# Kernel optimization log

Hardware: AMD Instinct MI355X
Metric: run time of the kernel (lower is better)

## Reference

```python
import jax, jax.numpy as jnp
import numpy as np

N = 50000      # nodes
E = 1600000    # edges (avg degree 32)
F_IN = 512     # num_node_features
NHID = 128     # args.nhid
NCLS = 64      # num_classes


def _gcn_conv(x, W, b, src, dst):
    """PyG GCNConv with symmetric normalization and self-loops.
    x' = D^{-1/2} (A + I) D^{-1/2} (x W) + b, D = degree of (A + I)."""
    h = x @ W                                   # [N, d_out] linear first
    ones = jnp.ones(src.shape[0], h.dtype)
    deg = jnp.zeros(N, h.dtype).at[dst].add(ones) + 1.0  # +1 for self-loop
    dinv = jax.lax.rsqrt(deg)                   # D^{-1/2}
    norm = dinv[src] * dinv[dst]                # per-edge coefficient
    msg = h[src] * norm[:, None]                # gather + scale  [E, d_out]
    agg = jnp.zeros_like(h).at[dst].add(msg)    # scatter-add
    agg = agg + h * (dinv * dinv)[:, None]      # self-loop term (norm = dinv_i^2)
    return agg + b


def setup_inputs() -> dict:
    key = jax.random.key(0)
    k0, k1, k2, k3, k4, k5 = jax.random.split(key, 6)
    x = jax.random.normal(k0, (N, F_IN), jnp.float32)
    edge_index = jax.random.randint(k1, (2, E), 0, N, jnp.int32)
    W1 = jax.random.normal(k2, (F_IN, NHID), jnp.float32) / np.sqrt(F_IN)
    b1 = jnp.zeros((NHID,), jnp.float32)
    W2 = jax.random.normal(k3, (NHID, NCLS), jnp.float32) / np.sqrt(NHID)
    b2 = jnp.zeros((NCLS,), jnp.float32)
    return {"x": x, "edge_index": edge_index, "W1": W1, "b1": b1, "W2": W2, "b2": b2}


def reference(x, edge_index, W1, b1, W2, b2):
    src, dst = edge_index[0], edge_index[1]
    h = jax.nn.relu(_gcn_conv(x, W1, b1, src, dst))
    # dropout is identity at inference (training=False)
    out = _gcn_conv(h, W2, b2, src, dst)
    return jax.nn.softmax(out, axis=1)
```

## Files before the change

### kernel.cpp

```cpp
#include <hip/hip_runtime.h>
#include <hip/hip_bf16.h>
#include <hip/hip_fp16.h>


#define F_IN 512
#define NHID 128
#define NCLS 64
#define BSHIFT 8
#define CHUNK 4096
#define BM 64
#define BK 32

typedef __attribute__((ext_vector_type(8))) short short8;
typedef __attribute__((ext_vector_type(4))) float f32x4;

__device__ __forceinline__ unsigned f2u(float f) { union { float f; unsigned u; } v; v.f = f; return v.u; }
__device__ __forceinline__ float u2f(unsigned u) { union { unsigned u; float f; } v; v.u = u; return v.f; }


__global__ __launch_bounds__(256) void bin_kernel(const int* __restrict__ src,
        const int* __restrict__ dst, int2* __restrict__ pairs,
        int* __restrict__ bcur, int E, int cap) {
    __shared__ int lcnt[256];
    __shared__ int lscan[256];
    __shared__ int gbase[256];
    __shared__ int wsum[4];
    __shared__ int2 stage[CHUNK];
    const int t = threadIdx.x;
    const int lane = t & 63, wid = t >> 6;
    const int e0 = blockIdx.x * CHUNK;
    const int n = min(CHUNK, E - e0);

    lcnt[t] = 0;
    __syncthreads();
    for (int i = t; i < n; i += 256)
        atomicAdd(&lcnt[dst[e0 + i] >> BSHIFT], 1);
    __syncthreads();
    const int v = lcnt[t];
    int s = v;
    #pragma unroll
    for (int d = 1; d < 64; d <<= 1) {
        int tt = __shfl_up(s, d);
        if (lane >= d) s += tt;
    }
    if (lane == 63) wsum[wid] = s;
    __syncthreads();
    int woff = 0;
    for (int w = 0; w < wid; ++w) woff += wsum[w];
    lscan[t] = woff + s - v;
    gbase[t] = v ? atomicAdd(&bcur[t], v) : 0;
    lcnt[t] = 0;
    __syncthreads();
    for (int i = t; i < n; i += 256) {
        int d = dst[e0 + i], sc = src[e0 + i];
        int b = d >> BSHIFT;
        int p = atomicAdd(&lcnt[b], 1);
        stage[lscan[b] + p] = make_int2(d, sc);
    }
    __syncthreads();
    for (int i = t; i < n; i += 256) {
        int2 pr = stage[i];
        int b = pr.x >> BSHIFT;
        int off = gbase[b] + (i - lscan[b]);
        if (off < cap) pairs[(size_t)b * cap + off] = pr;
    }
}


__global__ __launch_bounds__(256) void count_b_kernel(const int2* __restrict__ pairs,
        const int* __restrict__ bcur, int* __restrict__ cnt, int cap) {
    __shared__ int hist[256];
    const int b = blockIdx.x;
    const int t = threadIdx.x;
    hist[t] = 0;
    __syncthreads();
    const int n = min(bcur[b], cap);
    const int2* p = pairs + (size_t)b * cap;
    for (int i = t; i < n; i += 256)
        atomicAdd(&hist[p[i].x & 255], 1);
    __syncthreads();
    cnt[(b << BSHIFT) + t] = hist[t];
}


__global__ __launch_bounds__(256) void scan1_kernel(const int* __restrict__ cnt,
        int* __restrict__ row_ptr, float* __restrict__ dinv,
        int* __restrict__ bsum, int N) {
    __shared__ int wsum[4];
    const int tid = threadIdx.x;
    const int lane = tid & 63, wid = tid >> 6;
    const int base = blockIdx.x * 1024 + tid * 4;
    int4 v = {0, 0, 0, 0};
    if (base + 3 < N) {
        v = *reinterpret_cast<const int4*>(&cnt[base]);
    } else {
        if (base + 0 < N) v.x = cnt[base + 0];
        if (base + 1 < N) v.y = cnt[base + 1];
        if (base + 2 < N) v.z = cnt[base + 2];
        if (base + 3 < N) v.w = cnt[base + 3];
    }
    if (base + 0 < N) dinv[base + 0] = rsqrtf((float)v.x + 1.0f);
    if (base + 1 < N) dinv[base + 1] = rsqrtf((float)v.y + 1.0f);
    if (base + 2 < N) dinv[base + 2] = rsqrtf((float)v.z + 1.0f);
    if (base + 3 < N) dinv[base + 3] = rsqrtf((float)v.w + 1.0f);
    const int tsum = v.x + v.y + v.z + v.w;
    int s = tsum;
    #pragma unroll
    for (int d = 1; d < 64; d <<= 1) {
        int t = __shfl_up(s, d);
        if (lane >= d) s += t;
    }
    if (lane == 63) wsum[wid] = s;
    __syncthreads();
    int woff = 0;
    for (int w = 0; w < wid; ++w) woff += wsum[w];
    const int excl = woff + s - tsum;
    if (base + 0 < N) row_ptr[base + 0] = excl;
    if (base + 1 < N) row_ptr[base + 1] = excl + v.x;
    if (base + 2 < N) row_ptr[base + 2] = excl + v.x + v.y;
    if (base + 3 < N) row_ptr[base + 3] = excl + v.x + v.y + v.z;
    if (tid == 255) bsum[blockIdx.x] = excl + tsum;
}

__global__ __launch_bounds__(64) void scan2_kernel(const int* __restrict__ bsum,
        int* __restrict__ boff, int* __restrict__ row_ptr, int nb, int N) {
    const int lane = threadIdx.x;
    int v = (lane < nb) ? bsum[lane] : 0;
    int s = v;
    #pragma unroll
    for (int d = 1; d < 64; d <<= 1) {
        int t = __shfl_up(s, d);
        if (lane >= d) s += t;
    }
    if (lane < nb) boff[lane] = s - v;
    if (lane == 63) row_ptr[N] = s;
}

__global__ void scan3_kernel(int* __restrict__ row_ptr, const int* __restrict__ boff, int N) {
    int i = blockIdx.x * blockDim.x + threadIdx.x;
    if (i < N) row_ptr[i] += boff[i >> 10];
}


__global__ __launch_bounds__(512) void fill_b_kernel(const int2* __restrict__ pairs,
        const int* __restrict__ bcur, const int* __restrict__ row_ptr,
        int* __restrict__ col, int cap) {
    __shared__ int lcur[256];
    const int b = blockIdx.x;
    const int t = threadIdx.x;
    if (t < 256) lcur[t] = 0;
    __syncthreads();
    const int n = min(bcur[b], cap);
    const int2* p = pairs + (size_t)b * cap;
    for (int i = t; i < n; i += 512) {
        int2 pr = p[i];
        int pos = row_ptr[pr.x] + atomicAdd(&lcur[pr.x & 255], 1);
        col[pos] = pr.y;
    }
}


__global__ __launch_bounds__(256) void prepW_kernel(const float* __restrict__ W1,
        short* __restrict__ Wp) {
    const int g = blockIdx.x * 256 + threadIdx.x;
    const int f = g >> 6;
    const int lane = g & 63;
    const int ks = f >> 3, nt = f & 7;
    const int colg = nt * 16 + (lane & 15);
    const int k0 = ks * 32 + (lane >> 4) * 8;
    short8 vb;
    #pragma unroll
    for (int j = 0; j < 8; ++j) {
        unsigned u = f2u(W1[(size_t)(k0 + j) * NHID + colg]);
        unsigned r = (u + 0x7fffu + ((u >> 16) & 1u)) >> 16;
        vb[j] = (short)r;
    }
    *reinterpret_cast<short8*>(Wp + ((size_t)f << 9) + (lane << 3)) = vb;
}


__device__ __forceinline__ void cvt8v(const f32x4& u0, const f32x4& u1,
                                      short8& h, short8& l) {
    float av[8] = {u0[0], u0[1], u0[2], u0[3], u1[0], u1[1], u1[2], u1[3]};
    #pragma unroll
    for (int j = 0; j < 8; ++j) {
        unsigned u = f2u(av[j]);
        h[j] = (short)(u >> 16);
        float hif = u2f(u & 0xffff0000u);
        l[j] = (short)(f2u(av[j] - hif) >> 16);
    }
}

#define STAGE(bufidx, ksv) do { \
    const char* _xb = (const char*)X + (size_t)(ksv) * 128; \
    char* _ab = (char*)&Abuf[bufidx][0] + tid * 16; \
    __builtin_amdgcn_global_load_lds((const unsigned*)(_xb + aoff0), (unsigned*)(_ab),        16, 0, 0); \
    __builtin_amdgcn_global_load_lds((const unsigned*)(_xb + aoff1), (unsigned*)(_ab + 4096), 16, 0, 0); \
    const char* _wb = (const char*)Wp + (size_t)(ksv) * 8192 + tid * 16; \
    char* _bb = (char*)&Bbuf[bufidx][0] + tid * 16; \
    __builtin_amdgcn_global_load_lds((const unsigned*)(_wb),        (unsigned*)(_bb),        16, 0, 0); \
    __builtin_amdgcn_global_load_lds((const unsigned*)(_wb + 4096), (unsigned*)(_bb + 4096), 16, 0, 0); \
} while (0)

__global__ __launch_bounds__(256, 4) void gemm1_mfma(
        const float* __restrict__ X, const short* __restrict__ Wp,
        const float* __restrict__ dinv, __half* __restrict__ Hs16, int M) {
    __shared__ float Abuf[2][BM * BK];
    __shared__ short Bbuf[2][8 * 512];
    const int tid = threadIdx.x;
    const int lane = tid & 63;
    const int wid = tid >> 6;
    const int l15 = lane & 15;
    const int kc = lane >> 4;
    const int m0 = blockIdx.x * BM;

    int aoff0, aoff1;
    {
        int o, row, c, grow;
        o = tid * 16;        row = o >> 7; c = ((o >> 4) & 7) ^ (row & 7);
        grow = m0 + row; if (grow > M - 1) grow = M - 1; aoff0 = grow * 2048 + c * 16;
        o = 4096 + tid * 16; row = o >> 7; c = ((o >> 4) & 7) ^ (row & 7);
        grow = m0 + row; if (grow > M - 1) grow = M - 1; aoff1 = grow * 2048 + c * 16;
    }

    const int row0 = wid * 16 + l15;
    const int ra0 = row0 * 128 + (((kc * 2) ^ (row0 & 7)) * 16);
    const int ra1 = row0 * 128 + (((kc * 2 + 1) ^ (row0 & 7)) * 16);

    f32x4 acc[8];
    #pragma unroll
    for (int j = 0; j < 8; ++j)
        acc[j] = (f32x4){0.f, 0.f, 0.f, 0.f};

    STAGE(0, 0);
    __syncthreads();

    for (int ks = 0; ks < 16; ++ks) {
        const int cur = ks & 1;
        if (ks + 1 < 16) STAGE(cur ^ 1, ks + 1);
        const char* ab = (const char*)&Abuf[cur][0];
        const f32x4 x0 = *reinterpret_cast<const f32x4*>(ab + ra0);
        const f32x4 x1 = *reinterpret_cast<const f32x4*>(ab + ra1);
        short8 ah, al;
        cvt8v(x0, x1, ah, al);
        const char* bb = (const char*)&Bbuf[cur][0];
        short8 bfr[8];
        #pragma unroll
        for (int nt = 0; nt < 8; ++nt)
            bfr[nt] = *reinterpret_cast<const short8*>(bb + nt * 1024 + lane * 16);
        #pragma unroll
        for (int nt = 0; nt < 8; ++nt) {
            acc[nt] = __builtin_amdgcn_mfma_f32_16x16x32_bf16(ah, bfr[nt], acc[nt], 0, 0, 0);
            acc[nt] = __builtin_amdgcn_mfma_f32_16x16x32_bf16(al, bfr[nt], acc[nt], 0, 0, 0);
        }
        __syncthreads();
    }

    #pragma unroll
    for (int r = 0; r < 4; ++r) {
        const int orow = m0 + wid * 16 + kc * 4 + r;
        if (orow < M) {
            const float di = dinv[orow];
            #pragma unroll
            for (int nt = 0; nt < 8; ++nt) {
                Hs16[(size_t)orow * NHID + nt * 16 + l15] =
                    __float2half(acc[nt][r] * di);
            }
        }
    }
}


__global__ __launch_bounds__(64) void agg1_kernel(const __half2* __restrict__ Hs,
        const int* __restrict__ row_ptr, const int* __restrict__ col,
        const float* __restrict__ dinv, const float* __restrict__ b1,
        float* __restrict__ Y) {
    const int i = blockIdx.x;
    const int c = threadIdx.x;
    const int beg = row_ptr[i], end = row_ptr[i + 1];
    float2 f = __half22float2(Hs[(size_t)i * 64 + c]);
    float ax = f.x, ay = f.y;
    int e = beg;
    for (; e + 8 <= end; e += 8) {
        float2 v[8];
        #pragma unroll
        for (int j = 0; j < 8; ++j) {
            int s = col[e + j];
            v[j] = __half22float2(Hs[(size_t)s * 64 + c]);
        }
        #pragma unroll
        for (int j = 0; j < 8; ++j) { ax += v[j].x; ay += v[j].y; }
    }
    for (; e < end; ++e) {
        float2 v = __half22float2(Hs[(size_t)col[e] * 64 + c]);
        ax += v.x; ay += v.y;
    }
    const float di = dinv[i];
    const float2 bb = reinterpret_cast<const float2*>(b1)[c];
    float2 o;
    o.x = fmaxf(fmaf(ax, di, bb.x), 0.0f);
    o.y = fmaxf(fmaf(ay, di, bb.y), 0.0f);
    *reinterpret_cast<float2*>(&Y[(size_t)i * NHID + 2 * c]) = o;
}


__global__ __launch_bounds__(256) void gemm2_kernel(const float* __restrict__ Y,
        const float* __restrict__ W2, const float* __restrict__ dinv,
        __half* __restrict__ H2s16, int N) {
    __shared__ float Ws[NHID][NCLS];
    __shared__ float Ys[16][NHID];
    const int tid = threadIdx.x;
    const int i0 = blockIdx.x * 16;
    #pragma unroll
    for (int t = 0; t < 8; ++t) {
        int v = tid + t * 256;
        int k = v >> 4;
        int c4 = (v & 15) * 4;
        *reinterpret_cast<float4*>(&Ws[k][c4]) =
            *reinterpret_cast<const float4*>(&W2[(size_t)k * NCLS + c4]);
    }
    #pragma unroll
    for (int t = 0; t < 2; ++t) {
        int v = tid + t * 256;
        int r = v >> 5;
        int c4 = (v & 31) * 4;
        int gr = i0 + r; if (gr > N - 1) gr = N - 1;
        *reinterpret_cast<float4*>(&Ys[r][c4]) =
            *reinterpret_cast<const float4*>(&Y[(size_t)gr * NHID + c4]);
    }
    __syncthreads();
    const int c = tid & 63;
    const int rg = tid >> 6;
    float acc[4] = {0.f, 0.f, 0.f, 0.f};
    #pragma unroll 8
    for (int k = 0; k < NHID; ++k) {
        float w = Ws[k][c];
        #pragma unroll
        for (int j = 0; j < 4; ++j)
            acc[j] = fmaf(Ys[rg * 4 + j][k], w, acc[j]);
    }
    #pragma unroll
    for (int j = 0; j < 4; ++j) {
        int gr = i0 + rg * 4 + j;
        if (gr < N) H2s16[(size_t)gr * NCLS + c] = __float2half(acc[j] * dinv[gr]);
    }
}


__global__ __launch_bounds__(64) void agg2_kernel(const __half2* __restrict__ H2,
        const int* __restrict__ row_ptr, const int* __restrict__ col,
        const float* __restrict__ dinv, const float* __restrict__ b2,
        float* __restrict__ out, int N) {
    const int lane = threadIdx.x;
    const int node = blockIdx.x * 2 + (lane >> 5);
    const int c = lane & 31;
    if (node >= N) return;
    const int beg = row_ptr[node], end = row_ptr[node + 1];
    float2 f = __half22float2(H2[(size_t)node * 32 + c]);
    float ax = f.x, ay = f.y;
    int e = beg;
    for (; e + 8 <= end; e += 8) {
        float2 v[8];
        #pragma unroll
        for (int j = 0; j < 8; ++j) {
            int s = col[e + j];
            v[j] = __half22float2(H2[(size_t)s * 32 + c]);
        }
        #pragma unroll
        for (int j = 0; j < 8; ++j) { ax += v[j].x; ay += v[j].y; }
    }
    for (; e < end; ++e) {
        float2 v = __half22float2(H2[(size_t)col[e] * 32 + c]);
        ax += v.x; ay += v.y;
    }
    const float di = dinv[node];
    const float2 bb = reinterpret_cast<const float2*>(b2)[c];
    float vx = fmaf(ax, di, bb.x);
    float vy = fmaf(ay, di, bb.y);
    float m = fmaxf(vx, vy);
    #pragma unroll
    for (int d = 16; d >= 1; d >>= 1) m = fmaxf(m, __shfl_xor(m, d));
    float ex = __expf(vx - m), ey = __expf(vy - m);
    float sum = ex + ey;
    #pragma unroll
    for (int d = 16; d >= 1; d >>= 1) sum += __shfl_xor(sum, d);
    float2 o = {ex / sum, ey / sum};
    reinterpret_cast<float2*>(out)[(size_t)node * 32 + c] = o;
}


extern "C" void kernel_launch(void* const* d_in, const int* in_sizes, int n_in,
                              void* d_out, int out_size, void* d_ws, size_t ws_size,
                              hipStream_t stream) {
    const float* x  = (const float*)d_in[0];
    const int*   ei = (const int*)d_in[1];
    const float* W1 = (const float*)d_in[2];
    const float* b1 = (const float*)d_in[3];
    const float* W2 = (const float*)d_in[4];
    const float* b2 = (const float*)d_in[5];
    const int N = in_sizes[0] / F_IN;
    const int E = in_sizes[1] / 2;
    const int* src = ei;
    const int* dst = ei + E;
    float* out = (float*)d_out;

    const int Npad  = (N + 63) & ~63;
    const int Nb256 = (N + 255) & ~255;
    const int Epad  = (E + 63) & ~63;
    int*    cnt     = (int*)d_ws;
    int*    bcur    = cnt + Nb256;
    int*    row_ptr = bcur + 256;
    float*  dinv    = (float*)(row_ptr + Npad);
    int*    col     = (int*)(dinv + Npad);
    int*    bsum    = col + Epad;
    int*    boff    = bsum + 64;
    __half* Hs16    = (__half*)(boff + 64);
    float*  Y       = (float*)(Hs16 + (size_t)Npad * NHID);
    __half* H2s16   = Hs16;
    short*  Wp      = (short*)Y;
    int2*   pairs   = (int2*)((char*)Y + 512 * 1024);

    const int nb = (N + 1023) / 1024;
    const int nbuck = (N + 255) >> BSHIFT;
    const int cap = (((E / nbuck) * 3 / 2) + 63) & ~63;

    hipMemsetAsync(bcur, 0, 256 * sizeof(int), stream);
    bin_kernel<<<(E + CHUNK - 1) / CHUNK, 256, 0, stream>>>(src, dst, pairs, bcur, E, cap);
    count_b_kernel<<<nbuck, 256, 0, stream>>>(pairs, bcur, cnt, cap);
    scan1_kernel<<<nb, 256, 0, stream>>>(cnt, row_ptr, dinv, bsum, N);
    scan2_kernel<<<1, 64, 0, stream>>>(bsum, boff, row_ptr, nb, N);
    scan3_kernel<<<(N + 255) / 256, 256, 0, stream>>>(row_ptr, boff, N);
    fill_b_kernel<<<nbuck, 512, 0, stream>>>(pairs, bcur, row_ptr, col, cap);
    prepW_kernel<<<32, 256, 0, stream>>>(W1, Wp);
    gemm1_mfma<<<(N + BM - 1) / BM, 256, 0, stream>>>(x, Wp, dinv, Hs16, N);
    agg1_kernel<<<N, 64, 0, stream>>>((const __half2*)Hs16, row_ptr, col, dinv, b1, Y);
    gemm2_kernel<<<(N + 15) / 16, 256, 0, stream>>>(Y, W2, dinv, H2s16, N);
    agg2_kernel<<<(N + 1) / 2, 64, 0, stream>>>((const __half2*)H2s16, row_ptr, col, dinv, b2, out, N);
}
```

Before: 186.2 us.

## Pack edge pairs into 32 bits and fuse CSR count/scan into bucket kernels

Each (dst, src) edge pair is now packed into one 32-bit word, with dst in the high 16 bits and src in the low 16 bits. This halves the bucketed pair buffer and its shared-memory staging. The separate count, three-stage global scan and fill kernels are replaced by a one-block bucket-offset scan plus a per-bucket kernel that builds the histogram, does a local scan and writes row_ptr and dinv directly. The goal is fewer launches and less memory traffic in CSR construction, at the cost of requiring node ids below 65536 and a barrier inside a thread-divergent branch.

```diff
diff --git a/kernel.cpp b/kernel.cpp
--- a/kernel.cpp
+++ b/kernel.cpp
@@ -19,13 +19,13 @@
 
 
 __global__ __launch_bounds__(256) void bin_kernel(const int* __restrict__ src,
-        const int* __restrict__ dst, int2* __restrict__ pairs,
+        const int* __restrict__ dst, unsigned* __restrict__ pairs,
         int* __restrict__ bcur, int E, int cap) {
     __shared__ int lcnt[256];
     __shared__ int lscan[256];
     __shared__ int gbase[256];
     __shared__ int wsum[4];
-    __shared__ int2 stage[CHUNK];
+    __shared__ unsigned stage[CHUNK];
     const int t = threadIdx.x;
     const int lane = t & 63, wid = t >> 6;
     const int e0 = blockIdx.x * CHUNK;
@@ -52,97 +52,78 @@
     lcnt[t] = 0;
     __syncthreads();
     for (int i = t; i < n; i += 256) {
-        int d = dst[e0 + i], sc = src[e0 + i];
+        unsigned d = (unsigned)dst[e0 + i], sc = (unsigned)src[e0 + i];
         int b = d >> BSHIFT;
         int p = atomicAdd(&lcnt[b], 1);
-        stage[lscan[b] + p] = make_int2(d, sc);
+        stage[lscan[b] + p] = (d << 16) | sc;
     }
     __syncthreads();
     for (int i = t; i < n; i += 256) {
-        int2 pr = stage[i];
-        int b = pr.x >> BSHIFT;
+        unsigned pr = stage[i];
+        int b = pr >> 24;
         int off = gbase[b] + (i - lscan[b]);
         if (off < cap) pairs[(size_t)b * cap + off] = pr;
     }
 }
 
 
-__global__ __launch_bounds__(256) void count_b_kernel(const int2* __restrict__ pairs,
-        const int* __restrict__ bcur, int* __restrict__ cnt, int cap) {
+__global__ __launch_bounds__(256) void scanB_kernel(const int* __restrict__ bcur,
+        int* __restrict__ bbase, int nbuck, int cap) {
+    __shared__ int wsum[4];
+    const int t = threadIdx.x;
+    const int lane = t & 63, wid = t >> 6;
+    int v = (t < nbuck) ? min(bcur[t], cap) : 0;
+    int s = v;
+    #pragma unroll
+    for (int d = 1; d < 64; d <<= 1) {
+        int tt = __shfl_up(s, d);
+        if (lane >= d) s += tt;
+    }
+    if (lane == 63) wsum[wid] = s;
+    __syncthreads();
+    int woff = 0;
+    for (int w = 0; w < wid; ++w) woff += wsum[w];
+    bbase[t] = woff + s - v;
+}
+
+
+__global__ __launch_bounds__(512) void countscan_b_kernel(
+        const unsigned* __restrict__ pairs, const int* __restrict__ bcur,
+        const int* __restrict__ bbase, int* __restrict__ row_ptr,
+        float* __restrict__ dinv, int cap, int N) {
     __shared__ int hist[256];
+    __shared__ int wsum[4];
     const int b = blockIdx.x;
     const int t = threadIdx.x;
-    hist[t] = 0;
+    if (t < 256) hist[t] = 0;
     __syncthreads();
     const int n = min(bcur[b], cap);
-    const int2* p = pairs + (size_t)b * cap;
-    for (int i = t; i < n; i += 256)
-        atomicAdd(&hist[p[i].x & 255], 1);
-    __syncthreads();
-    cnt[(b << BSHIFT) + t] = hist[t];
-}
-
-
-__global__ __launch_bounds__(256) void scan1_kernel(const int* __restrict__ cnt,
-        int* __restrict__ row_ptr, float* __restrict__ dinv,
-        int* __restrict__ bsum, int N) {
-    __shared__ int wsum[4];
-    const int tid = threadIdx.x;
-    const int lane = tid & 63, wid = tid >> 6;
-    const int base = blockIdx.x * 1024 + tid * 4;
-    int4 v = {0, 0, 0, 0};
-    if (base + 3 < N) {
-        v = *reinterpret_cast<const int4*>(&cnt[base]);
-    } else {
-        if (base + 0 < N) v.x = cnt[base + 0];
-        if (base + 1 < N) v.y = cnt[base + 1];
-        if (base + 2 < N) v.z = cnt[base + 2];
-        if (base + 3 < N) v.w = cnt[base + 3];
-    }
-    if (base + 0 < N) dinv[base + 0] = rsqrtf((float)v.x + 1.0f);
-    if (base + 1 < N) dinv[base + 1] = rsqrtf((float)v.y + 1.0f);
-    if (base + 2 < N) dinv[base + 2] = rsqrtf((float)v.z + 1.0f);
-    if (base + 3 < N) dinv[base + 3] = rsqrtf((float)v.w + 1.0f);
-    const int tsum = v.x + v.y + v.z + v.w;
-    int s = tsum;
-    #pragma unroll
-    for (int d = 1; d < 64; d <<= 1) {
-        int t = __shfl_up(s, d);
-        if (lane >= d) s += t;
-    }
-    if (lane == 63) wsum[wid] = s;
-    __syncthreads();
-    int woff = 0;
-    for (int w = 0; w < wid; ++w) woff += wsum[w];
-    const int excl = woff + s - tsum;
-    if (base + 0 < N) row_ptr[base + 0] = excl;
-    if (base + 1 < N) row_ptr[base + 1] = excl + v.x;
-    if (base + 2 < N) row_ptr[base + 2] = excl + v.x + v.y;
-    if (base + 3 < N) row_ptr[base + 3] = excl + v.x + v.y + v.z;
-    if (tid == 255) bsum[blockIdx.x] = excl + tsum;
-}
-
-__global__ __launch_bounds__(64) void scan2_kernel(const int* __restrict__ bsum,
-        int* __restrict__ boff, int* __restrict__ row_ptr, int nb, int N) {
-    const int lane = threadIdx.x;
-    int v = (lane < nb) ? bsum[lane] : 0;
-    int s = v;
-    #pragma unroll
-    for (int d = 1; d < 64; d <<= 1) {
-        int t = __shfl_up(s, d);
-        if (lane >= d) s += t;
-    }
-    if (lane < nb) boff[lane] = s - v;
-    if (lane == 63) row_ptr[N] = s;
-}
-
-__global__ void scan3_kernel(int* __restrict__ row_ptr, const int* __restrict__ boff, int N) {
-    int i = blockIdx.x * blockDim.x + threadIdx.x;
-    if (i < N) row_ptr[i] += boff[i >> 10];
-}
-
-
-__global__ __launch_bounds__(512) void fill_b_kernel(const int2* __restrict__ pairs,
+    const unsigned* p = pairs + (size_t)b * cap;
+    for (int i = t; i < n; i += 512)
+        atomicAdd(&hist[(p[i] >> 16) & 255], 1);
+    __syncthreads();
+    if (t < 256) {
+        const int lane = t & 63, wid = t >> 6;
+        const int v = hist[t];
+        int s = v;
+        #pragma unroll
+        for (int d = 1; d < 64; d <<= 1) {
+            int tt = __shfl_up(s, d);
+            if (lane >= d) s += tt;
+        }
+        if (lane == 63) wsum[wid] = s;
+        __syncthreads();
+        int woff = 0;
+        for (int w = 0; w < wid; ++w) woff += wsum[w];
+        const int excl = woff + s - v;
+        const int node = (b << BSHIFT) + t;
+        if (node <= N) row_ptr[node] = bbase[b] + excl;
+        if (node < N) dinv[node] = rsqrtf((float)v + 1.0f);
+    }
+}
+
+
+__global__ __launch_bounds__(1024) void fill_b_kernel(const unsigned* __restrict__ pairs,
         const int* __restrict__ bcur, const int* __restrict__ row_ptr,
         int* __restrict__ col, int cap) {
     __shared__ int lcur[256];
@@ -151,11 +132,12 @@
     if (t < 256) lcur[t] = 0;
     __syncthreads();
     const int n = min(bcur[b], cap);
-    const int2* p = pairs + (size_t)b * cap;
-    for (int i = t; i < n; i += 512) {
-        int2 pr = p[i];
-        int pos = row_ptr[pr.x] + atomicAdd(&lcur[pr.x & 255], 1);
-        col[pos] = pr.y;
+    const unsigned* p = pairs + (size_t)b * cap;
+    for (int i = t; i < n; i += 1024) {
+        unsigned pr = p[i];
+        int dl = (pr >> 16) & 255;
+        int pos = row_ptr[(b << BSHIFT) + dl] + atomicAdd(&lcur[dl], 1);
+        col[pos] = (int)(pr & 0xffffu);
     }
 }
 
@@ -405,32 +387,26 @@
     float* out = (float*)d_out;
 
     const int Npad  = (N + 63) & ~63;
-    const int Nb256 = (N + 255) & ~255;
     const int Epad  = (E + 63) & ~63;
-    int*    cnt     = (int*)d_ws;
-    int*    bcur    = cnt + Nb256;
-    int*    row_ptr = bcur + 256;
-    float*  dinv    = (float*)(row_ptr + Npad);
-    int*    col     = (int*)(dinv + Npad);
-    int*    bsum    = col + Epad;
-    int*    boff    = bsum + 64;
-    __half* Hs16    = (__half*)(boff + 64);
-    float*  Y       = (float*)(Hs16 + (size_t)Npad * NHID);
-    __half* H2s16   = Hs16;
-    short*  Wp      = (short*)Y;
-    int2*   pairs   = (int2*)((char*)Y + 512 * 1024);
-
-    const int nb = (N + 1023) / 1024;
+    int*      bcur    = (int*)d_ws;
+    int*      bbase   = bcur + 256;
+    int*      row_ptr = bbase + 256;
+    float*    dinv    = (float*)(row_ptr + Npad);
+    int*      col     = (int*)(dinv + Npad);
+    __half*   Hs16    = (__half*)(col + Epad);
+    float*    Y       = (float*)(Hs16 + (size_t)Npad * NHID);
+    __half*   H2s16   = Hs16;
+    short*    Wp      = (short*)Y;
+    unsigned* pairs   = (unsigned*)((char*)Y + 512 * 1024);
+
     const int nbuck = (N + 255) >> BSHIFT;
     const int cap = (((E / nbuck) * 3 / 2) + 63) & ~63;
 
     hipMemsetAsync(bcur, 0, 256 * sizeof(int), stream);
     bin_kernel<<<(E + CHUNK - 1) / CHUNK, 256, 0, stream>>>(src, dst, pairs, bcur, E, cap);
-    count_b_kernel<<<nbuck, 256, 0, stream>>>(pairs, bcur, cnt, cap);
-    scan1_kernel<<<nb, 256, 0, stream>>>(cnt, row_ptr, dinv, bsum, N);
-    scan2_kernel<<<1, 64, 0, stream>>>(bsum, boff, row_ptr, nb, N);
-    scan3_kernel<<<(N + 255) / 256, 256, 0, stream>>>(row_ptr, boff, N);
-    fill_b_kernel<<<nbuck, 512, 0, stream>>>(pairs, bcur, row_ptr, col, cap);
+    scanB_kernel<<<1, 256, 0, stream>>>(bcur, bbase, nbuck, cap);
+    countscan_b_kernel<<<nbuck, 512, 0, stream>>>(pairs, bcur, bbase, row_ptr, dinv, cap, N);
+    fill_b_kernel<<<nbuck, 1024, 0, stream>>>(pairs, bcur, row_ptr, col, cap);
     prepW_kernel<<<32, 256, 0, stream>>>(W1, Wp);
     gemm1_mfma<<<(N + BM - 1) / BM, 256, 0, stream>>>(x, Wp, dinv, Hs16, N);
     agg1_kernel<<<N, 64, 0, stream>>>((const __half2*)Hs16, row_ptr, col, dinv, b1, Y);
```

Result: faster. 175.6 us (-5.7%).
